# Kernel tuning notes

Measured on AMD Instinct MI355X. Metric: run time of the kernel, lower is better.

Reference implementation:

```python
import jax, jax.numpy as jnp
import numpy as np

N_DIM = 64          # n (output dim of h); d_h_in == n since traj_input=False
HIDDEN = 512        # layer_width
N_LAYERS = 3        # n_hidden_layers
BATCH = 4096


def setup_inputs() -> dict:
    key = jax.random.key(0)
    ks = jax.random.split(key, 7)
    s = 1.0 / np.sqrt(HIDDEN)
    return {
        "x": jax.random.normal(ks[0], (BATCH, 3 * N_DIM), dtype=jnp.float32),
        "W_in": jax.random.normal(ks[1], (HIDDEN, N_DIM), dtype=jnp.float32) / np.sqrt(N_DIM),
        "b_in": jax.random.normal(ks[2], (HIDDEN,), dtype=jnp.float32) * 0.01,
        "W_h": jax.random.normal(ks[3], (N_LAYERS, HIDDEN, HIDDEN), dtype=jnp.float32) * s,
        "b_h": jax.random.normal(ks[4], (N_LAYERS, HIDDEN), dtype=jnp.float32) * 0.01,
        "W_out": jax.random.normal(ks[5], (N_DIM, HIDDEN), dtype=jnp.float32) * s,
        "b_out": jax.random.normal(ks[6], (N_DIM,), dtype=jnp.float32) * 0.01,
    }


def _branch(xin, W_in, b_in, W_h, b_h, W_out, b_out):
    """Replicates the MLP forward + the module's hand-rolled Jacobian chain.
    Note: faithfully reproduces the original's delta masks, which re-apply
    layer ii to its own (already-activated) output h[ii+1]."""
    hs = [xin @ W_in.T + b_in]                      # h[0]: [B, H]
    for ii in range(N_LAYERS):
        hs.append(jax.nn.relu(hs[-1] @ W_h[ii].T + b_h[ii]))
    out = hs[-1] @ W_out.T + b_out                  # [B, n]

    g = (W_h[0] @ W_in)                             # [H, d]
    delta = (hs[1] @ W_h[0].T + b_h[0] > 0).astype(xin.dtype)  # sign(relu(.))
    g = delta[:, :, None] * g[None, :, :]           # [B, H, d]
    for ii in range(1, N_LAYERS):
        g = jnp.einsum("hk,bkd->bhd", W_h[ii], g)
        delta = (hs[ii + 1] @ W_h[ii].T + b_h[ii] > 0).astype(xin.dtype)
        g = delta[:, :, None] * g
    g = jnp.einsum("nh,bhd->bnd", W_out, g)         # [B, n, d]
    return out, g


def reference(x, W_in, b_in, W_h, b_h, W_out, b_out):
    d = N_DIM
    xt, xtdot, x_zero = x[:, :d], x[:, d:2 * d], x[:, 2 * d:]

    h_out, h_grad = _branch(xt, W_in, b_in, W_h, b_h, W_out, b_out)
    h_dot = jnp.einsum("bnd,bd->bn", h_grad, xtdot)

    _, h_zerograd = _branch(x_zero, W_in, b_in, W_h, b_h, W_out, b_out)
    h_zerograd = h_zerograd[:, :, :d]               # no-op here (d_h_in == n)
    zng = jnp.sqrt(jnp.sum(h_zerograd * h_zerograd, axis=2))  # L2 norm over dim 2

    return jnp.concatenate([h_out, h_dot, zng], axis=1)       # [B, 3n]
```

## Files before the change

kernel.cpp:

```cpp
#include <hip/hip_runtime.h>
#include <math.h>

typedef __attribute__((ext_vector_type(8))) short s8v;
typedef __attribute__((ext_vector_type(4))) short s4v;
typedef __attribute__((ext_vector_type(4))) float f4v;
typedef __attribute__((ext_vector_type(16))) float f16v;

static __device__ __forceinline__ unsigned short f2bf(float f) {
    union { float f; unsigned int u; } v; v.f = f;
    unsigned int r = v.u + 0x7fffu + ((v.u >> 16) & 1u);
    return (unsigned short)(r >> 16);
}
static __device__ __forceinline__ float bf2f(unsigned short h) {
    union { unsigned int u; float f; } t; t.u = ((unsigned int)h) << 16;
    return t.f;
}

__global__ void conv_g0(const float* __restrict__ Win, const float* __restrict__ Wh,
                        const float* __restrict__ Wout,
                        unsigned short* __restrict__ whi, unsigned short* __restrict__ wlo,
                        unsigned short* __restrict__ G0hi, unsigned short* __restrict__ G0lo,
                        unsigned short* __restrict__ G0F) {
    if (blockIdx.x < 3328) {
        int i = blockIdx.x * 256 + threadIdx.x;
        float v;
        if (i < 32768)       v = Win[i];
        else if (i < 819200) v = Wh[i - 32768];
        else                 v = Wout[i - 819200];
        unsigned short h = f2bf(v);
        whi[i] = h;
        wlo[i] = f2bf(v - bf2f(h));
    } else {
        int i = (blockIdx.x - 3328) * 4 + (threadIdx.x >> 6);
        int j = threadIdx.x & 63;
        float acc = 0.f;
        for (int k = 0; k < 512; ++k)
            acc = fmaf(Wh[i * 512 + k], Win[k * 64 + j], acc);
        unsigned short h = f2bf(acc);
        G0hi[i * 64 + j] = h;
        G0lo[i * 64 + j] = f2bf(acc - bf2f(h));
        int sl = ((i >> 4) * 2 + (j >> 5)) * 64 + (j & 31) + 32 * ((i >> 3) & 1);
        G0F[(size_t)sl * 8 + (i & 7)] = h;
    }
}


#define DF_LOAD(k0)                                                              \
    {                                                                            \
        _Pragma("unroll")                                                        \
        for (int r = 0; r < 2; ++r) {                                            \
            int idx = tid + r * 512;                                             \
            int row = idx >> 3, kq = (idx & 7) * 4;                              \
            xr[r] = *(const float4*)(X + (size_t)(m0 + row) * ldx + (k0) + kq);  \
        }                                                                        \
        {                                                                        \
            int row = tid >> 3, kq = (tid & 7) * 4;                              \
            wr = *(const float4*)(W + (size_t)(n0 + row) * ldw + (k0) + kq);     \
        }                                                                        \
    }
#define DF_STASH()                                                               \
    {                                                                            \
        _Pragma("unroll")                                                        \
        for (int r = 0; r < 2; ++r) {                                            \
            int idx = tid + r * 512;                                             \
            int row = idx >> 3, kq = (idx & 7) * 4;                              \
            Xs[kq + 0][row] = xr[r].x; Xs[kq + 1][row] = xr[r].y;                \
            Xs[kq + 2][row] = xr[r].z; Xs[kq + 3][row] = xr[r].w;                \
        }                                                                        \
        {                                                                        \
            int row = tid >> 3, kq = (tid & 7) * 4;                              \
            Ws[kq + 0][row] = wr.x; Ws[kq + 1][row] = wr.y;                      \
            Ws[kq + 2][row] = wr.z; Ws[kq + 3][row] = wr.w;                      \
        }                                                                        \
    }

static __device__ __forceinline__ void dual_fp32_body(
    unsigned char* lds, const float* __restrict__ X, int ldx,
    const float* __restrict__ W, int ldw, const float* __restrict__ bias,
    float* __restrict__ C, int ldc, unsigned char* __restrict__ maskOut,
    const unsigned char* __restrict__ maskMul, int K, int N, int mode,
    int m0, int n0)
{
    const int tid = threadIdx.x;
    float (*Xs)[132] = (float(*)[132])lds;
    float (*Ws)[68]  = (float(*)[68])(lds + 16896);
    const int tx = tid & 15, ty = tid >> 4;
    float acc[4][4] = {};
    float4 xr[2], wr;

    DF_LOAD(0);
    DF_STASH();
    __syncthreads();

    for (int k0 = 0; k0 < K; k0 += 32) {
        bool last = (k0 + 32 >= K);
        if (!last) DF_LOAD(k0 + 32);
        #pragma unroll
        for (int kk = 0; kk < 32; ++kk) {
            float4 a0 = *(const float4*)&Xs[kk][ty * 4];
            float4 b0 = *(const float4*)&Ws[kk][tx * 4];
            float av[4] = {a0.x, a0.y, a0.z, a0.w};
            float bv[4] = {b0.x, b0.y, b0.z, b0.w};
            #pragma unroll
            for (int i = 0; i < 4; ++i)
                #pragma unroll
                for (int j = 0; j < 4; ++j)
                    acc[i][j] = fmaf(av[i], bv[j], acc[i][j]);
        }
        __syncthreads();
        if (!last) {
            DF_STASH();
            __syncthreads();
        }
    }

    float4 bb = {0, 0, 0, 0};
    if (mode & 1) bb = *(const float4*)(bias + n0 + tx * 4);
    const int c0 = n0 + tx * 4;
    #pragma unroll
    for (int i = 0; i < 4; ++i) {
        int r = m0 + ty * 4 + i;
        float v[4];
        #pragma unroll
        for (int j = 0; j < 4; ++j) {
            v[j] = acc[i][j];
            if (mode & 1) v[j] += ((const float*)&bb)[j];
        }
        if (mode & 8) {
            uchar4 mo;
            mo.x = v[0] > 0.0f; mo.y = v[1] > 0.0f; mo.z = v[2] > 0.0f; mo.w = v[3] > 0.0f;
            *(uchar4*)&maskOut[(size_t)r * N + c0] = mo;
        }
        if (mode & 16) {
            uchar4 mm = *(const uchar4*)&maskMul[(size_t)r * N + c0];
            v[0] *= mm.x; v[1] *= mm.y; v[2] *= mm.z; v[3] *= mm.w;
        }
        if (mode & 2) {
            #pragma unroll
            for (int j = 0; j < 4; ++j) v[j] = fmaxf(v[j], 0.0f);
        }
        if (mode & 4) {
            float4 st = {v[0], v[1], v[2], v[3]};
            *(float4*)(C + (size_t)r * ldc + c0) = st;
        }
    }
}
#undef DF_LOAD
#undef DF_STASH

#define DM_LOAD(k0)                                                                \
    {                                                                              \
        _Pragma("unroll")                                                          \
        for (int r = 0; r < 2; ++r) {                                              \
            int idx = tid + r * 512;                                               \
            int row = idx >> 3, kq = (idx & 7) * 4;                                \
            xr[r] = *(const float4*)(X + (size_t)(m0 + row) * ldx + (k0) + kq);    \
        }                                                                          \
        if (wload) {                                                               \
            int row = tid >> 2, kc = (tid & 3) * 8;                                \
            wh = *(const s8v*)(Whi + (size_t)(n0 + row) * ldw + (k0) + kc);        \
            wl = *(const s8v*)(Wlo + (size_t)(n0 + row) * ldw + (k0) + kc);        \
        }                                                                          \
    }
#define DM_STASH()                                                                 \
    {                                                                              \
        _Pragma("unroll")                                                          \
        for (int r = 0; r < 2; ++r) {                                              \
            int idx = tid + r * 512;                                               \
            int row = idx >> 3, kq = (idx & 7) * 4;                                \
            float a[4] = {xr[r].x, xr[r].y, xr[r].z, xr[r].w};                     \
            s4v hv, lv;                                                            \
            _Pragma("unroll")                                                      \
            for (int j = 0; j < 4; ++j) {                                          \
                unsigned short h = f2bf(a[j]);                                     \
                hv[j] = (short)h;                                                  \
                lv[j] = (short)f2bf(a[j] - bf2f(h));                               \
            }                                                                      \
            *(s4v*)&Xh[row * 40 + kq] = hv;                                        \
            *(s4v*)&Xl[row * 40 + kq] = lv;                                        \
        }                                                                          \
        if (wload) {                                                               \
            int row = tid >> 2, kc = (tid & 3) * 8;                                \
            *(s8v*)&Wsh[row * 40 + kc] = wh;                                       \
            *(s8v*)&Wsl[row * 40 + kc] = wl;                                       \
        }                                                                          \
    }

static __device__ __forceinline__ void dual_mfma_body(
    unsigned char* lds, const float* __restrict__ X, int ldx,
    const unsigned short* __restrict__ Whi, const unsigned short* __restrict__ Wlo, int ldw,
    const float* __restrict__ bias, float* __restrict__ C, int ldc,
    unsigned char* __restrict__ maskOut, const unsigned char* __restrict__ maskMul,
    int K, int N, int mode, int m0, int n0)
{
    const int tid = threadIdx.x;
    unsigned short* Xh  = (unsigned short*)lds;
    unsigned short* Xl  = (unsigned short*)(lds + 10240);
    unsigned short* Wsh = (unsigned short*)(lds + 20480);
    unsigned short* Wsl = (unsigned short*)(lds + 25600);

    const int wave = tid >> 6, lane = tid & 63;
    const int q = lane >> 4, ln = lane & 15;
    const int wm = (wave & 3) * 32;
    const int wn = (wave >> 2) * 32;

    f4v acc[2][2];
    #pragma unroll
    for (int mt = 0; mt < 2; ++mt)
        #pragma unroll
        for (int nt = 0; nt < 2; ++nt)
            acc[mt][nt] = (f4v)(0.0f);

    float4 xr[2];
    s8v wh, wl;
    const bool wload = (tid < 256);

    DM_LOAD(0);
    DM_STASH();
    __syncthreads();

    for (int k0 = 0; k0 < K; k0 += 32) {
        bool last = (k0 + 32 >= K);
        if (!last) DM_LOAD(k0 + 32);

        s8v ah[2], al[2], bh[2], bl[2];
        #pragma unroll
        for (int mt = 0; mt < 2; ++mt) {
            int rowm = wm + mt * 16 + ln;
            ah[mt] = *(const s8v*)&Xh[rowm * 40 + q * 8];
            al[mt] = *(const s8v*)&Xl[rowm * 40 + q * 8];
        }
        #pragma unroll
        for (int nt = 0; nt < 2; ++nt) {
            int rown = wn + nt * 16 + ln;
            bh[nt] = *(const s8v*)&Wsh[rown * 40 + q * 8];
            bl[nt] = *(const s8v*)&Wsl[rown * 40 + q * 8];
        }
        #pragma unroll
        for (int mt = 0; mt < 2; ++mt)
            #pragma unroll
            for (int nt = 0; nt < 2; ++nt) {
                acc[mt][nt] = __builtin_amdgcn_mfma_f32_16x16x32_bf16(ah[mt], bh[nt], acc[mt][nt], 0, 0, 0);
                acc[mt][nt] = __builtin_amdgcn_mfma_f32_16x16x32_bf16(ah[mt], bl[nt], acc[mt][nt], 0, 0, 0);
                acc[mt][nt] = __builtin_amdgcn_mfma_f32_16x16x32_bf16(al[mt], bh[nt], acc[mt][nt], 0, 0, 0);
            }

        __syncthreads();
        if (!last) {
            DM_STASH();
            __syncthreads();
        }
    }

    #pragma unroll
    for (int nt = 0; nt < 2; ++nt) {
        int n = n0 + wn + nt * 16 + ln;
        float bv = (mode & 1) ? bias[n] : 0.0f;
        #pragma unroll
        for (int mt = 0; mt < 2; ++mt) {
            int mbase = m0 + wm + mt * 16 + q * 4;
            #pragma unroll
            for (int r = 0; r < 4; ++r) {
                int m = mbase + r;
                float v = acc[mt][nt][r] + bv;
                if (mode & 8)  maskOut[(size_t)m * N + n] = (v > 0.0f) ? 1 : 0;
                if (mode & 16) v *= (float)maskMul[(size_t)m * N + n];
                if (mode & 2)  v = fmaxf(v, 0.0f);
                if (mode & 4)  C[(size_t)m * ldc + n] = v;
            }
        }
    }
}
#undef DM_LOAD
#undef DM_STASH

__global__ __launch_bounds__(512) void h0_pack(
    const float* __restrict__ x, const float* __restrict__ Win,
    const unsigned short* __restrict__ WinH, const unsigned short* __restrict__ WinL,
    const float* __restrict__ bin, float* __restrict__ tA, float* __restrict__ zA,
    const unsigned short* __restrict__ whi,
    unsigned short* __restrict__ WhF, unsigned short* __restrict__ WoF)
{
    __shared__ __align__(16) unsigned char lds[30720];
    const int m0 = blockIdx.x * 128, n0 = blockIdx.y * 64;
    int z = blockIdx.z;
    if (z == 0)
        dual_fp32_body(lds, x, 192, Win, 64, bin, tA, 512, 0, 0, 64, 512, 1 | 4, m0, n0);
    else if (z == 1)
        dual_mfma_body(lds, x + 128, 192, WinH, WinL, 64, bin, zA, 512, 0, 0, 64, 512, 1 | 4, m0, n0);
    else {
        int i = (blockIdx.y * 32 + blockIdx.x) * 512 + threadIdx.x;
        if (i < 65536) {
            int lane = i & 63, ks = (i >> 6) & 31, g32 = (i >> 11) & 15, s = i >> 15;
            int row = g32 * 32 + (lane & 31);
            int k   = ks * 16 + (lane >> 5) * 8;
            const unsigned short* src = whi + 294912 + (size_t)s * 262144 + row * 512 + k;
            *(s8v*)(WhF + (size_t)i * 8) = *(const s8v*)src;
        } else if (i < 65536 + 4096) {
            int j = i - 65536;
            int lane = j & 63, ks = (j >> 6) & 31, g32 = j >> 11;
            int row = g32 * 32 + (lane & 31);
            int k   = ks * 16 + (lane >> 5) * 8;
            const unsigned short* src = whi + 819200 + row * 512 + k;
            *(s8v*)(WoF + (size_t)j * 8) = *(const s8v*)src;
        }
    }
}

__global__ __launch_bounds__(512) void gemm_dualM(
    const float* __restrict__ X0, const float* __restrict__ X1, int ldx,
    const float* __restrict__ W, int ldw,
    const unsigned short* __restrict__ Whi, const unsigned short* __restrict__ Wlo,
    const float* __restrict__ bias,
    float* __restrict__ C0, float* __restrict__ C1, int ldc,
    unsigned char* __restrict__ mo0, unsigned char* __restrict__ mo1,
    int K, int N, int mode)
{
    __shared__ __align__(16) unsigned char lds[30720];
    const int m0 = blockIdx.x * 128, n0 = blockIdx.y * 64;
    if (blockIdx.z == 0)
        dual_fp32_body(lds, X0, ldx, W, ldw, bias, C0, ldc, mo0, 0, K, N, mode, m0, n0);
    else
        dual_mfma_body(lds, X1, ldx, Whi, Wlo, ldw, bias, C1, ldc, mo1, 0, K, N, mode, m0, n0);
}

__global__ __launch_bounds__(512) void gemm_dual4(
    const float* __restrict__ X0, const float* __restrict__ X1, int ldx,
    const float* __restrict__ Wn, const float* __restrict__ Wd, int ldw,
    const unsigned short* __restrict__ WnH, const unsigned short* __restrict__ WnL,
    const unsigned short* __restrict__ WdH, const unsigned short* __restrict__ WdL,
    const float* __restrict__ bn, const float* __restrict__ bd,
    float* __restrict__ C0, float* __restrict__ C1, int ldc,
    unsigned char* __restrict__ mot, unsigned char* __restrict__ moz,
    int K, int N)
{
    __shared__ __align__(16) unsigned char lds[30720];
    const int m0 = blockIdx.x * 128, n0 = blockIdx.y * 64;
    int z = blockIdx.z;
    if (z == 0)
        dual_fp32_body(lds, X0, ldx, Wn, ldw, bn, C0, ldc, 0, 0, K, N, 1 | 2 | 4, m0, n0);
    else if (z == 2)
        dual_fp32_body(lds, X0, ldx, Wd, ldw, bd, 0, ldc, mot, 0, K, N, 1 | 8, m0, n0);
    else if (z == 1)
        dual_mfma_body(lds, X1, ldx, WnH, WnL, ldw, bn, C1, ldc, 0, 0, K, N, 1 | 2 | 4, m0, n0);
    else
        dual_mfma_body(lds, X1, ldx, WdH, WdL, ldw, bd, 0, ldc, moz, 0, K, N, 1 | 8, m0, n0);
}

__global__ __launch_bounds__(512) void d3v1(
    const float* __restrict__ tB, const float* __restrict__ zB, const float* __restrict__ x,
    const float* __restrict__ Wh2,
    const unsigned short* __restrict__ Wh2H, const unsigned short* __restrict__ Wh2L,
    const unsigned short* __restrict__ G0hi, const unsigned short* __restrict__ G0lo,
    const float* __restrict__ bh2, float* __restrict__ tA,
    unsigned char* __restrict__ mt3, unsigned char* __restrict__ mz3,
    const unsigned char* __restrict__ mt1)
{
    __shared__ __align__(16) unsigned char lds[30720];
    const int m0 = blockIdx.x * 128, n0 = blockIdx.y * 64;
    int z = blockIdx.z;
    if (z == 0)
        dual_fp32_body(lds, tB, 512, Wh2, 512, bh2, 0, 512, mt3, 0, 512, 512, 1 | 8, m0, n0);
    else if (z == 1)
        dual_mfma_body(lds, zB, 512, Wh2H, Wh2L, 512, bh2, 0, 512, mz3, 0, 512, 512, 1 | 8, m0, n0);
    else
        dual_mfma_body(lds, x + 64, 192, G0hi, G0lo, 64, 0, tA, 512, 0, mt1, 64, 512, 4 | 16, m0, n0);
}

__global__ __launch_bounds__(512) void gemm_m1(
    const float* __restrict__ X, int ldx,
    const unsigned short* __restrict__ Whi, const unsigned short* __restrict__ Wlo, int ldw,
    float* __restrict__ C, int ldc,
    const unsigned char* __restrict__ maskMul,
    int K, int N, int mode)
{
    __shared__ __align__(16) unsigned char lds[30720];
    dual_mfma_body(lds, X, ldx, Whi, Wlo, ldw, 0, C, ldc, 0, maskMul, K, N, mode,
                   blockIdx.x * 128, blockIdx.y * 64);
}

__global__ __launch_bounds__(512) void gemm_mm(
    const float* __restrict__ X0, const float* __restrict__ X1, int ldx,
    const unsigned short* __restrict__ Whi, const unsigned short* __restrict__ Wlo, int ldw,
    const float* __restrict__ bias,
    float* __restrict__ C0, float* __restrict__ C1, int ldc,
    int K, int N, int mode0, int mode1)
{
    __shared__ __align__(16) unsigned char lds[30720];
    const int m0 = blockIdx.x * 128, n0 = blockIdx.y * 64;
    if (blockIdx.z == 0)
        dual_mfma_body(lds, X0, ldx, Whi, Wlo, ldw, bias, C0, ldc, 0, 0, K, N, mode0, m0, n0);
    else
        dual_mfma_body(lds, X1, ldx, Whi, Wlo, ldw, bias, C1, ldc, 0, 0, K, N, mode1, m0, n0);
}

__global__ __launch_bounds__(512, 4) void zng_v2(
    const unsigned short* __restrict__ WhF,
    const unsigned short* __restrict__ WoF,
    const unsigned short* __restrict__ G0F,
    const unsigned char* __restrict__ mz1,
    const unsigned char* __restrict__ mz2,
    const unsigned char* __restrict__ mz3,
    float* __restrict__ out,
    const float* __restrict__ tA,
    const unsigned short* __restrict__ Wh1H, const unsigned short* __restrict__ Wh1L,
    const unsigned char* __restrict__ mt2,
    float* __restrict__ zA)
{
    __shared__ __align__(16) unsigned char ldsb[66560];

    if (blockIdx.x >= 4096) {
        int idx = blockIdx.x - 4096;
        dual_mfma_body(ldsb, tA, 512, Wh1H, Wh1L, 512, 0, zA, 512, 0, mt2,
                       512, 512, 4 | 16, (idx & 31) * 128, (idx >> 5) * 64);
        return;
    }

    unsigned short* RtF = (unsigned short*)ldsb;
    unsigned char* m2s = ldsb + 65536;
    unsigned char* m3s = ldsb + 66048;

    const int b0  = blockIdx.x;
    const int tid = threadIdx.x;

    m2s[tid] = mz2[(size_t)b0 * 512 + tid];
    m3s[tid] = mz3[(size_t)b0 * 512 + tid];

    #pragma unroll
    for (int it = 0; it < 8; ++it) {
        int sl = it * 512 + tid;
        int ls = sl & 63;
        int ks = sl >> 7;
        int k0 = ks * 16 + (ls >> 5) * 8;
        s8v g = *(const s8v*)(G0F + (size_t)sl * 8);
        const unsigned char* mm = mz1 + (size_t)b0 * 512 + k0;
        unsigned int mlo = *(const unsigned int*)(mm);
        unsigned int mhi = *(const unsigned int*)(mm + 4);
        s8v r;
        #pragma unroll
        for (int j = 0; j < 4; ++j) r[j] = ((mlo >> (8 * j)) & 1) ? g[j] : (short)0;
        #pragma unroll
        for (int j = 0; j < 4; ++j) r[4 + j] = ((mhi >> (8 * j)) & 1) ? g[4 + j] : (short)0;
        *(s8v*)(&RtF[(size_t)sl * 8]) = r;
    }
    __syncthreads();

    const int lane = tid & 63, wave = tid >> 6;
    const int l31 = lane & 31, h = lane >> 5;

    for (int s = 0; s < 2; ++s) {
        const unsigned short* Ar0 = WhF + (size_t)s * 262144
                                  + (size_t)(wave * 2) * 16384 + lane * 8;
        const unsigned short* Ar1 = Ar0 + 16384;

        f16v acc[2][2];
        #pragma unroll
        for (int mt = 0; mt < 2; ++mt)
            #pragma unroll
            for (int nt = 0; nt < 2; ++nt)
                acc[mt][nt] = (f16v)(0.0f);

        s8v a0A = *(const s8v*)(Ar0);
        s8v a1A = *(const s8v*)(Ar1);
        s8v a0B = *(const s8v*)(Ar0 + 512);
        s8v a1B = *(const s8v*)(Ar1 + 512);
        s8v b0c = *(const s8v*)&RtF[lane * 8];
        s8v b1c = *(const s8v*)&RtF[512 + lane * 8];

        #pragma unroll 4
        for (int ks = 0; ks < 32; ++ks) {
            int kf = ((ks + 2) & 31) * 512;
            s8v a0N = *(const s8v*)(Ar0 + kf);
            s8v a1N = *(const s8v*)(Ar1 + kf);
            int kb = ((ks + 1) & 31) * 1024;
            s8v b0n = *(const s8v*)&RtF[kb + lane * 8];
            s8v b1n = *(const s8v*)&RtF[kb + 512 + lane * 8];

            __builtin_amdgcn_s_setprio(1);
            acc[0][0] = __builtin_amdgcn_mfma_f32_32x32x16_bf16(a0A, b0c, acc[0][0], 0, 0, 0);
            acc[0][1] = __builtin_amdgcn_mfma_f32_32x32x16_bf16(a0A, b1c, acc[0][1], 0, 0, 0);
            acc[1][0] = __builtin_amdgcn_mfma_f32_32x32x16_bf16(a1A, b0c, acc[1][0], 0, 0, 0);
            acc[1][1] = __builtin_amdgcn_mfma_f32_32x32x16_bf16(a1A, b1c, acc[1][1], 0, 0, 0);
            __builtin_amdgcn_s_setprio(0);

            a0A = a0B; a0B = a0N;
            a1A = a1B; a1B = a1N;
            b0c = b0n; b1c = b1n;
        }
        __syncthreads();

        const unsigned char* msk = (s == 0) ? m2s : m3s;
        #pragma unroll
        for (int mt = 0; mt < 2; ++mt) {
            #pragma unroll
            for (int g = 0; g < 4; ++g) {
                int kk = wave * 64 + mt * 32 + g * 8 + h * 4;
                int ks = wave * 4 + mt * 2 + (g >> 1);
                int khalf = g & 1;
                uchar4 mv = *(const uchar4*)&msk[kk];
                unsigned char mb[4] = {mv.x, mv.y, mv.z, mv.w};
                #pragma unroll
                for (int nt = 0; nt < 2; ++nt) {
                    s4v pk;
                    #pragma unroll
                    for (int r = 0; r < 4; ++r) {
                        float v = mb[r] ? acc[mt][nt][g * 4 + r] : 0.0f;
                        pk[r] = (short)f2bf(v);
                    }
                    *(s4v*)(&RtF[(ks * 2 + nt) * 512 + (l31 + 32 * khalf) * 8 + h * 4]) = pk;
                }
            }
        }
        __syncthreads();
    }

    if (wave < 2) {
        const unsigned short* Wr = WoF + wave * 16384 + lane * 8;
        f16v a3[2];
        a3[0] = (f16v)(0.0f);
        a3[1] = (f16v)(0.0f);
        #pragma unroll 2
        for (int ks = 0; ks < 32; ++ks) {
            s8v af = *(const s8v*)(Wr + ks * 512);
            s8v bb0 = *(const s8v*)&RtF[ks * 1024 + lane * 8];
            s8v bb1 = *(const s8v*)&RtF[ks * 1024 + 512 + lane * 8];
            a3[0] = __builtin_amdgcn_mfma_f32_32x32x16_bf16(af, bb0, a3[0], 0, 0, 0);
            a3[1] = __builtin_amdgcn_mfma_f32_32x32x16_bf16(af, bb1, a3[1], 0, 0, 0);
        }
        float sq[16];
        #pragma unroll
        for (int i = 0; i < 16; ++i) {
            float v0 = a3[0][i], v1 = a3[1][i];
            sq[i] = fmaf(v0, v0, v1 * v1);
        }
        #pragma unroll
        for (int off = 1; off < 32; off <<= 1)
            #pragma unroll
            for (int i = 0; i < 16; ++i)
                sq[i] += __shfl_xor(sq[i], off, 64);
        if (l31 == 0) {
            #pragma unroll
            for (int g = 0; g < 4; ++g)
                #pragma unroll
                for (int r = 0; r < 4; ++r)
                    out[(size_t)b0 * 192 + 128 + wave * 32 + g * 8 + h * 4 + r] = sqrtf(sq[g * 4 + r]);
        }
    }
}

extern "C" void kernel_launch(void* const* d_in, const int* in_sizes, int n_in,
                              void* d_out, int out_size, void* d_ws, size_t ws_size,
                              hipStream_t stream) {
    const float* x    = (const float*)d_in[0];
    const float* Win  = (const float*)d_in[1];
    const float* bin  = (const float*)d_in[2];
    const float* Wh   = (const float*)d_in[3];
    const float* bh   = (const float*)d_in[4];
    const float* Wout = (const float*)d_in[5];
    const float* bout = (const float*)d_in[6];
    float* out = (float*)d_out;

    char* ws = (char*)d_ws;
    unsigned short* whi  = (unsigned short*)(ws);
    unsigned short* wlo  = (unsigned short*)(ws + 1703936);
    unsigned short* G0hi = (unsigned short*)(ws + 3407872);
    unsigned short* G0lo = (unsigned short*)(ws + 3473408);
    unsigned short* G0F  = (unsigned short*)(ws + 3538944);
    unsigned char*  masks = (unsigned char*)(ws + 3604480);
    unsigned char* mt1 = masks + 0 * 2097152;
    unsigned char* mt2 = masks + 1 * 2097152;
    unsigned char* mt3 = masks + 2 * 2097152;
    unsigned char* mz1 = masks + 3 * 2097152;
    unsigned char* mz2 = masks + 4 * 2097152;
    unsigned char* mz3 = masks + 5 * 2097152;
    float* bufs = (float*)(ws + 3604480 + 12582912);
    float* tA = bufs + 0 * 2097152;
    float* tB = bufs + 1 * 2097152;
    float* zA = bufs + 2 * 2097152;
    float* zB = bufs + 3 * 2097152;
    unsigned short* WhF = (unsigned short*)(ws + 49741824);
    unsigned short* WoF = (unsigned short*)(ws + 50790400);

    const unsigned short* WinH  = whi,          *WinL  = wlo;
    const unsigned short* Wh0H  = whi + 32768,  *Wh0L  = wlo + 32768;
    const unsigned short* Wh1H  = whi + 294912, *Wh1L  = wlo + 294912;
    const unsigned short* Wh2H  = whi + 557056, *Wh2L  = wlo + 557056;
    const unsigned short* WoutH = whi + 819200, *WoutL = wlo + 819200;

    const float* Wh0 = Wh;
    const float* Wh1 = Wh + 262144;
    const float* Wh2 = Wh + 524288;
    const float* bh0 = bh, *bh1 = bh + 512, *bh2 = bh + 1024;

    conv_g0<<<dim3(3456), dim3(256), 0, stream>>>(Win, Wh, Wout, whi, wlo, G0hi, G0lo, G0F);
    h0_pack<<<dim3(32, 8, 3), dim3(512), 0, stream>>>(x, Win, WinH, WinL, bin, tA, zA,
                                                      whi, WhF, WoF);

    gemm_dualM<<<dim3(32, 8, 2), dim3(512), 0, stream>>>(tA, zA, 512, Wh0, 512, Wh0H, Wh0L, bh0,
                                                         tB, zB, 512, 0, 0, 512, 512, 1 | 2 | 4);
    gemm_dual4<<<dim3(32, 8, 4), dim3(512), 0, stream>>>(tB, zB, 512, Wh1, Wh0, 512,
                                                         Wh1H, Wh1L, Wh0H, Wh0L, bh1, bh0,
                                                         tA, zA, 512, mt1, mz1, 512, 512);
    gemm_dual4<<<dim3(32, 8, 4), dim3(512), 0, stream>>>(tA, zA, 512, Wh2, Wh1, 512,
                                                         Wh2H, Wh2L, Wh1H, Wh1L, bh2, bh1,
                                                         tB, zB, 512, mt2, mz2, 512, 512);
    d3v1<<<dim3(32, 8, 3), dim3(512), 0, stream>>>(tB, zB, x, Wh2, Wh2H, Wh2L, G0hi, G0lo,
                                                   bh2, tA, mt3, mz3, mt1);

    zng_v2<<<dim3(4352), dim3(512), 0, stream>>>(WhF, WoF, G0F, mz1, mz2, mz3, out,
                                                 tA, Wh1H, Wh1L, mt2, zA);

    gemm_m1<<<dim3(32, 8), dim3(512), 0, stream>>>(zA, 512, Wh2H, Wh2L, 512, zB, 512,
                                                   mt3, 512, 512, 4 | 16);

    gemm_mm<<<dim3(32, 1, 2), dim3(512), 0, stream>>>(tB, zB, 512, WoutH, WoutL, 512, bout,
                                                      out, out + 64, 192, 512, 64, 1 | 4, 4);
}
```

Before: 662.0 us.

## Process two batch rows per zng block to reuse weight fragments

The per-sample Jacobian-norm kernel now handles two batch samples per 512-thread block. Each group of four waves owns one sample and computes 128 rows of the 512x64 product with four M-tiles, so every loaded weight fragment feeds twice as many MFMAs. LDS per block doubles to about 130 KB and the launch-bounds occupancy hint drops from 4 to 2, which cuts resident waves and raises register pressure in exchange for halving global weight traffic per sample.

```diff
diff --git a/kernel.cpp b/kernel.cpp
--- a/kernel.cpp
+++ b/kernel.cpp
@@ -394,7 +394,7 @@
         dual_mfma_body(lds, X1, ldx, Whi, Wlo, ldw, bias, C1, ldc, 0, 0, K, N, mode1, m0, n0);
 }
 
-__global__ __launch_bounds__(512, 4) void zng_v2(
+__global__ __launch_bounds__(512, 2) void zng_v2(
     const unsigned short* __restrict__ WhF,
     const unsigned short* __restrict__ WoF,
     const unsigned short* __restrict__ G0F,
@@ -407,95 +407,113 @@
     const unsigned char* __restrict__ mt2,
     float* __restrict__ zA)
 {
-    __shared__ __align__(16) unsigned char ldsb[66560];
-
-    if (blockIdx.x >= 4096) {
-        int idx = blockIdx.x - 4096;
+    __shared__ __align__(16) unsigned char ldsb[133120];
+
+    if (blockIdx.x >= 2048) {
+        int idx = blockIdx.x - 2048;
         dual_mfma_body(ldsb, tA, 512, Wh1H, Wh1L, 512, 0, zA, 512, 0, mt2,
                        512, 512, 4 | 16, (idx & 31) * 128, (idx >> 5) * 64);
         return;
     }
 
-    unsigned short* RtF = (unsigned short*)ldsb;
-    unsigned char* m2s = ldsb + 65536;
-    unsigned char* m3s = ldsb + 66048;
+    unsigned short* RtF0 = (unsigned short*)ldsb;
+    unsigned short* RtF1 = (unsigned short*)(ldsb + 65536);
+    unsigned char* m2s = ldsb + 131072;
+    unsigned char* m3s = ldsb + 132096;
 
     const int b0  = blockIdx.x;
     const int tid = threadIdx.x;
 
-    m2s[tid] = mz2[(size_t)b0 * 512 + tid];
-    m3s[tid] = mz3[(size_t)b0 * 512 + tid];
-
     #pragma unroll
-    for (int it = 0; it < 8; ++it) {
-        int sl = it * 512 + tid;
-        int ls = sl & 63;
-        int ks = sl >> 7;
-        int k0 = ks * 16 + (ls >> 5) * 8;
-        s8v g = *(const s8v*)(G0F + (size_t)sl * 8);
-        const unsigned char* mm = mz1 + (size_t)b0 * 512 + k0;
-        unsigned int mlo = *(const unsigned int*)(mm);
-        unsigned int mhi = *(const unsigned int*)(mm + 4);
-        s8v r;
-        #pragma unroll
-        for (int j = 0; j < 4; ++j) r[j] = ((mlo >> (8 * j)) & 1) ? g[j] : (short)0;
-        #pragma unroll
-        for (int j = 0; j < 4; ++j) r[4 + j] = ((mhi >> (8 * j)) & 1) ? g[4 + j] : (short)0;
-        *(s8v*)(&RtF[(size_t)sl * 8]) = r;
+    for (int e = 0; e < 2; ++e) {
+        m2s[e * 512 + tid] = mz2[(size_t)(2 * b0 + e) * 512 + tid];
+        m3s[e * 512 + tid] = mz3[(size_t)(2 * b0 + e) * 512 + tid];
+    }
+
+    {
+        const int e = tid >> 8, t256 = tid & 255;
+        unsigned short* RtF = e ? RtF1 : RtF0;
+        const unsigned char* mme = mz1 + (size_t)(2 * b0 + e) * 512;
+        #pragma unroll
+        for (int it = 0; it < 16; ++it) {
+            int sl = it * 256 + t256;
+            int ls = sl & 63;
+            int ks = sl >> 7;
+            int k0 = ks * 16 + (ls >> 5) * 8;
+            s8v g = *(const s8v*)(G0F + (size_t)sl * 8);
+            unsigned int mlo = *(const unsigned int*)(mme + k0);
+            unsigned int mhi = *(const unsigned int*)(mme + k0 + 4);
+            s8v r;
+            #pragma unroll
+            for (int j = 0; j < 4; ++j) r[j] = ((mlo >> (8 * j)) & 1) ? g[j] : (short)0;
+            #pragma unroll
+            for (int j = 0; j < 4; ++j) r[4 + j] = ((mhi >> (8 * j)) & 1) ? g[4 + j] : (short)0;
+            *(s8v*)(&RtF[(size_t)sl * 8]) = r;
+        }
     }
     __syncthreads();
 
     const int lane = tid & 63, wave = tid >> 6;
     const int l31 = lane & 31, h = lane >> 5;
+    const int we = wave >> 2;
+    const int wq = wave & 3;
+    unsigned short* RtF = we ? RtF1 : RtF0;
 
     for (int s = 0; s < 2; ++s) {
-        const unsigned short* Ar0 = WhF + (size_t)s * 262144
-                                  + (size_t)(wave * 2) * 16384 + lane * 8;
-        const unsigned short* Ar1 = Ar0 + 16384;
-
-        f16v acc[2][2];
-        #pragma unroll
-        for (int mt = 0; mt < 2; ++mt)
+        const unsigned short* Ar = WhF + (size_t)s * 262144
+                                 + (size_t)(wq * 4) * 16384 + lane * 8;
+
+        f16v acc[4][2];
+        #pragma unroll
+        for (int mt = 0; mt < 4; ++mt)
             #pragma unroll
             for (int nt = 0; nt < 2; ++nt)
                 acc[mt][nt] = (f16v)(0.0f);
 
-        s8v a0A = *(const s8v*)(Ar0);
-        s8v a1A = *(const s8v*)(Ar1);
-        s8v a0B = *(const s8v*)(Ar0 + 512);
-        s8v a1B = *(const s8v*)(Ar1 + 512);
+        s8v aA[4], aB[4];
+        #pragma unroll
+        for (int mt = 0; mt < 4; ++mt) {
+            aA[mt] = *(const s8v*)(Ar + (size_t)mt * 16384);
+            aB[mt] = *(const s8v*)(Ar + (size_t)mt * 16384 + 512);
+        }
         s8v b0c = *(const s8v*)&RtF[lane * 8];
         s8v b1c = *(const s8v*)&RtF[512 + lane * 8];
 
         #pragma unroll 4
         for (int ks = 0; ks < 32; ++ks) {
             int kf = ((ks + 2) & 31) * 512;
-            s8v a0N = *(const s8v*)(Ar0 + kf);
-            s8v a1N = *(const s8v*)(Ar1 + kf);
+            s8v aN[4];
+            #pragma unroll
+            for (int mt = 0; mt < 4; ++mt)
+                aN[mt] = *(const s8v*)(Ar + (size_t)mt * 16384 + kf);
             int kb = ((ks + 1) & 31) * 1024;
             s8v b0n = *(const s8v*)&RtF[kb + lane * 8];
             s8v b1n = *(const s8v*)&RtF[kb + 512 + lane * 8];
 
             __builtin_amdgcn_s_setprio(1);
-            acc[0][0] = __builtin_amdgcn_mfma_f32_32x32x16_bf16(a0A, b0c, acc[0][0], 0, 0, 0);
-            acc[0][1] = __builtin_amdgcn_mfma_f32_32x32x16_bf16(a0A, b1c, acc[0][1], 0, 0, 0);
-            acc[1][0] = __builtin_amdgcn_mfma_f32_32x32x16_bf16(a1A, b0c, acc[1][0], 0, 0, 0);
-            acc[1][1] = __builtin_amdgcn_mfma_f32_32x32x16_bf16(a1A, b1c, acc[1][1], 0, 0, 0);
+            #pragma unroll
+            for (int mt = 0; mt < 4; ++mt) {
+                acc[mt][0] = __builtin_amdgcn_mfma_f32_32x32x16_bf16(aA[mt], b0c, acc[mt][0], 0, 0, 0);
+                acc[mt][1] = __builtin_amdgcn_mfma_f32_32x32x16_bf16(aA[mt], b1c, acc[mt][1], 0, 0, 0);
+            }
             __builtin_amdgcn_s_setprio(0);
 
-            a0A = a0B; a0B = a0N;
-            a1A = a1B; a1B = a1N;
+            #pragma unroll
+            for (int mt = 0; mt < 4; ++mt) {
+                aA[mt] = aB[mt];
+                aB[mt] = aN[mt];
+            }
             b0c = b0n; b1c = b1n;
         }
         __syncthreads();
 
-        const unsigned char* msk = (s == 0) ? m2s : m3s;
-        #pragma unroll
-        for (int mt = 0; mt < 2; ++mt) {
+        const unsigned char* msk = ((s == 0) ? m2s : m3s) + we * 512;
+        #pragma unroll
+        for (int mt = 0; mt < 4; ++mt) {
             #pragma unroll
             for (int g = 0; g < 4; ++g) {
-                int kk = wave * 64 + mt * 32 + g * 8 + h * 4;
-                int ks = wave * 4 + mt * 2 + (g >> 1);
+                int kk = wq * 128 + mt * 32 + g * 8 + h * 4;
+                int ks2 = wq * 8 + mt * 2 + (g >> 1);
                 int khalf = g & 1;
                 uchar4 mv = *(const uchar4*)&msk[kk];
                 unsigned char mb[4] = {mv.x, mv.y, mv.z, mv.w};
@@ -507,15 +525,15 @@
                         float v = mb[r] ? acc[mt][nt][g * 4 + r] : 0.0f;
                         pk[r] = (short)f2bf(v);
                     }
-                    *(s4v*)(&RtF[(ks * 2 + nt) * 512 + (l31 + 32 * khalf) * 8 + h * 4]) = pk;
+                    *(s4v*)(&RtF[(ks2 * 2 + nt) * 512 + (l31 + 32 * khalf) * 8 + h * 4]) = pk;
                 }
             }
         }
         __syncthreads();
     }
 
-    if (wave < 2) {
-        const unsigned short* Wr = WoF + wave * 16384 + lane * 8;
+    if (wq < 2) {
+        const unsigned short* Wr = WoF + wq * 16384 + lane * 8;
         f16v a3[2];
         a3[0] = (f16v)(0.0f);
         a3[1] = (f16v)(0.0f);
@@ -543,7 +561,7 @@
             for (int g = 0; g < 4; ++g)
                 #pragma unroll
                 for (int r = 0; r < 4; ++r)
-                    out[(size_t)b0 * 192 + 128 + wave * 32 + g * 8 + h * 4 + r] = sqrtf(sq[g * 4 + r]);
+                    out[(size_t)(2 * b0 + we) * 192 + 128 + wq * 32 + g * 8 + h * 4 + r] = sqrtf(sq[g * 4 + r]);
         }
     }
 }
@@ -607,7 +625,7 @@
     d3v1<<<dim3(32, 8, 3), dim3(512), 0, stream>>>(tB, zB, x, Wh2, Wh2H, Wh2L, G0hi, G0lo,
                                                    bh2, tA, mt3, mz3, mt1);
 
-    zng_v2<<<dim3(4352), dim3(512), 0, stream>>>(WhF, WoF, G0F, mz1, mz2, mz3, out,
+    zng_v2<<<dim3(2304), dim3(512), 0, stream>>>(WhF, WoF, G0F, mz1, mz2, mz3, out,
                                                  tA, Wh1H, Wh1L, mt2, zA);
 
     gemm_m1<<<dim3(32, 8), dim3(512), 0, stream>>>(zA, 512, Wh2H, Wh2L, 512, zB, 512,
```

Result: slower. 698.5 us (+5.5%).

## Store intermediate activations as pre-split bf16 hi/lo pairs between GEMM stages

Applied to the files above, without the earlier changes.

Producer GEMM epilogues now write bf16 hi/lo split pairs instead of fp32 for the activation and tangent buffers consumed by split-bf16 MFMA GEMMs. A new pp_mfma_body loads these pre-split operands directly, which removes the per-tile fp32-to-bf16 split work in the load path. Global traffic per element stays the same (two shorts instead of one float), but the split conversion moves from every consumer tile into one producer epilogue. The scalar 2-byte epilogue stores may be less coalesced than the previous 4-byte stores.

```diff
diff --git a/kernel.cpp b/kernel.cpp
--- a/kernel.cpp
+++ b/kernel.cpp
@@ -148,6 +148,37 @@
 #undef DF_LOAD
 #undef DF_STASH
 
+static __device__ __forceinline__ void mfma_epi(
+    f4v (&acc)[2][2], const float* __restrict__ bias,
+    float* __restrict__ C, unsigned short* __restrict__ Ch, unsigned short* __restrict__ Cl,
+    int ldc, unsigned char* __restrict__ maskOut, const unsigned char* __restrict__ maskMul,
+    int N, int mode, int m0, int n0, int wm, int wn, int q, int ln)
+{
+    #pragma unroll
+    for (int nt = 0; nt < 2; ++nt) {
+        int n = n0 + wn + nt * 16 + ln;
+        float bv = (mode & 1) ? bias[n] : 0.0f;
+        #pragma unroll
+        for (int mt = 0; mt < 2; ++mt) {
+            int mbase = m0 + wm + mt * 16 + q * 4;
+            #pragma unroll
+            for (int r = 0; r < 4; ++r) {
+                int m = mbase + r;
+                float v = acc[mt][nt][r] + bv;
+                if (mode & 8)  maskOut[(size_t)m * N + n] = (v > 0.0f) ? 1 : 0;
+                if (mode & 16) v *= (float)maskMul[(size_t)m * N + n];
+                if (mode & 2)  v = fmaxf(v, 0.0f);
+                if (mode & 4)  C[(size_t)m * ldc + n] = v;
+                if (mode & 32) {
+                    unsigned short hh = f2bf(v);
+                    Ch[(size_t)m * ldc + n] = hh;
+                    Cl[(size_t)m * ldc + n] = f2bf(v - bf2f(hh));
+                }
+            }
+        }
+    }
+}
+
 #define DM_LOAD(k0)                                                                \
     {                                                                              \
         _Pragma("unroll")                                                          \
@@ -189,8 +220,9 @@
 static __device__ __forceinline__ void dual_mfma_body(
     unsigned char* lds, const float* __restrict__ X, int ldx,
     const unsigned short* __restrict__ Whi, const unsigned short* __restrict__ Wlo, int ldw,
-    const float* __restrict__ bias, float* __restrict__ C, int ldc,
-    unsigned char* __restrict__ maskOut, const unsigned char* __restrict__ maskMul,
+    const float* __restrict__ bias,
+    float* __restrict__ C, unsigned short* __restrict__ Ch, unsigned short* __restrict__ Cl,
+    int ldc, unsigned char* __restrict__ maskOut, const unsigned char* __restrict__ maskMul,
     int K, int N, int mode, int m0, int n0)
 {
     const int tid = threadIdx.x;
@@ -252,32 +284,109 @@
         }
     }
 
-    #pragma unroll
-    for (int nt = 0; nt < 2; ++nt) {
-        int n = n0 + wn + nt * 16 + ln;
-        float bv = (mode & 1) ? bias[n] : 0.0f;
-        #pragma unroll
-        for (int mt = 0; mt < 2; ++mt) {
-            int mbase = m0 + wm + mt * 16 + q * 4;
-            #pragma unroll
-            for (int r = 0; r < 4; ++r) {
-                int m = mbase + r;
-                float v = acc[mt][nt][r] + bv;
-                if (mode & 8)  maskOut[(size_t)m * N + n] = (v > 0.0f) ? 1 : 0;
-                if (mode & 16) v *= (float)maskMul[(size_t)m * N + n];
-                if (mode & 2)  v = fmaxf(v, 0.0f);
-                if (mode & 4)  C[(size_t)m * ldc + n] = v;
-            }
-        }
-    }
+    mfma_epi(acc, bias, C, Ch, Cl, ldc, maskOut, maskMul, N, mode, m0, n0, wm, wn, q, ln);
 }
 #undef DM_LOAD
 #undef DM_STASH
+
+#define PP_LOAD(k0)                                                                \
+    {                                                                              \
+        int row = tid >> 2, kc = (tid & 3) * 8;                                    \
+        xh8 = *(const s8v*)(Xhg + (size_t)(m0 + row) * ldx + (k0) + kc);           \
+        xl8 = *(const s8v*)(Xlg + (size_t)(m0 + row) * ldx + (k0) + kc);           \
+        if (wload) {                                                               \
+            wh = *(const s8v*)(Whi + (size_t)(n0 + row) * ldw + (k0) + kc);        \
+            wl = *(const s8v*)(Wlo + (size_t)(n0 + row) * ldw + (k0) + kc);        \
+        }                                                                          \
+    }
+#define PP_STASH()                                                                 \
+    {                                                                              \
+        int row = tid >> 2, kc = (tid & 3) * 8;                                    \
+        *(s8v*)&Xh[row * 40 + kc] = xh8;                                           \
+        *(s8v*)&Xl[row * 40 + kc] = xl8;                                           \
+        if (wload) {                                                               \
+            *(s8v*)&Wsh[row * 40 + kc] = wh;                                       \
+            *(s8v*)&Wsl[row * 40 + kc] = wl;                                       \
+        }                                                                          \
+    }
+
+static __device__ __forceinline__ void pp_mfma_body(
+    unsigned char* lds,
+    const unsigned short* __restrict__ Xhg, const unsigned short* __restrict__ Xlg, int ldx,
+    const unsigned short* __restrict__ Whi, const unsigned short* __restrict__ Wlo, int ldw,
+    const float* __restrict__ bias,
+    float* __restrict__ C, unsigned short* __restrict__ Ch, unsigned short* __restrict__ Cl,
+    int ldc, unsigned char* __restrict__ maskOut, const unsigned char* __restrict__ maskMul,
+    int K, int N, int mode, int m0, int n0)
+{
+    const int tid = threadIdx.x;
+    unsigned short* Xh  = (unsigned short*)lds;
+    unsigned short* Xl  = (unsigned short*)(lds + 10240);
+    unsigned short* Wsh = (unsigned short*)(lds + 20480);
+    unsigned short* Wsl = (unsigned short*)(lds + 25600);
+
+    const int wave = tid >> 6, lane = tid & 63;
+    const int q = lane >> 4, ln = lane & 15;
+    const int wm = (wave & 3) * 32;
+    const int wn = (wave >> 2) * 32;
+
+    f4v acc[2][2];
+    #pragma unroll
+    for (int mt = 0; mt < 2; ++mt)
+        #pragma unroll
+        for (int nt = 0; nt < 2; ++nt)
+            acc[mt][nt] = (f4v)(0.0f);
+
+    s8v xh8, xl8, wh, wl;
+    const bool wload = (tid < 256);
+
+    PP_LOAD(0);
+    PP_STASH();
+    __syncthreads();
+
+    for (int k0 = 0; k0 < K; k0 += 32) {
+        bool last = (k0 + 32 >= K);
+        if (!last) PP_LOAD(k0 + 32);
+
+        s8v ah[2], al[2], bh[2], bl[2];
+        #pragma unroll
+        for (int mt = 0; mt < 2; ++mt) {
+            int rowm = wm + mt * 16 + ln;
+            ah[mt] = *(const s8v*)&Xh[rowm * 40 + q * 8];
+            al[mt] = *(const s8v*)&Xl[rowm * 40 + q * 8];
+        }
+        #pragma unroll
+        for (int nt = 0; nt < 2; ++nt) {
+            int rown = wn + nt * 16 + ln;
+            bh[nt] = *(const s8v*)&Wsh[rown * 40 + q * 8];
+            bl[nt] = *(const s8v*)&Wsl[rown * 40 + q * 8];
+        }
+        #pragma unroll
+        for (int mt = 0; mt < 2; ++mt)
+            #pragma unroll
+            for (int nt = 0; nt < 2; ++nt) {
+                acc[mt][nt] = __builtin_amdgcn_mfma_f32_16x16x32_bf16(ah[mt], bh[nt], acc[mt][nt], 0, 0, 0);
+                acc[mt][nt] = __builtin_amdgcn_mfma_f32_16x16x32_bf16(ah[mt], bl[nt], acc[mt][nt], 0, 0, 0);
+                acc[mt][nt] = __builtin_amdgcn_mfma_f32_16x16x32_bf16(al[mt], bh[nt], acc[mt][nt], 0, 0, 0);
+            }
+
+        __syncthreads();
+        if (!last) {
+            PP_STASH();
+            __syncthreads();
+        }
+    }
+
+    mfma_epi(acc, bias, C, Ch, Cl, ldc, maskOut, maskMul, N, mode, m0, n0, wm, wn, q, ln);
+}
+#undef PP_LOAD
+#undef PP_STASH
 
 __global__ __launch_bounds__(512) void h0_pack(
     const float* __restrict__ x, const float* __restrict__ Win,
     const unsigned short* __restrict__ WinH, const unsigned short* __restrict__ WinL,
-    const float* __restrict__ bin, float* __restrict__ tA, float* __restrict__ zA,
+    const float* __restrict__ bin, float* __restrict__ tA,
+    unsigned short* __restrict__ zAh, unsigned short* __restrict__ zAl,
     const unsigned short* __restrict__ whi,
     unsigned short* __restrict__ WhF, unsigned short* __restrict__ WoF)
 {
@@ -287,7 +396,8 @@
     if (z == 0)
         dual_fp32_body(lds, x, 192, Win, 64, bin, tA, 512, 0, 0, 64, 512, 1 | 4, m0, n0);
     else if (z == 1)
-        dual_mfma_body(lds, x + 128, 192, WinH, WinL, 64, bin, zA, 512, 0, 0, 64, 512, 1 | 4, m0, n0);
+        dual_mfma_body(lds, x + 128, 192, WinH, WinL, 64, bin, 0, zAh, zAl, 512, 0, 0,
+                       64, 512, 1 | 32, m0, n0);
     else {
         int i = (blockIdx.y * 32 + blockIdx.x) * 512 + threadIdx.x;
         if (i < 65536) {
@@ -308,51 +418,58 @@
 }
 
 __global__ __launch_bounds__(512) void gemm_dualM(
-    const float* __restrict__ X0, const float* __restrict__ X1, int ldx,
-    const float* __restrict__ W, int ldw,
+    const float* __restrict__ X0,
+    const unsigned short* __restrict__ X1h, const unsigned short* __restrict__ X1l,
+    const float* __restrict__ W,
     const unsigned short* __restrict__ Whi, const unsigned short* __restrict__ Wlo,
     const float* __restrict__ bias,
-    float* __restrict__ C0, float* __restrict__ C1, int ldc,
-    unsigned char* __restrict__ mo0, unsigned char* __restrict__ mo1,
-    int K, int N, int mode)
+    float* __restrict__ C0,
+    unsigned short* __restrict__ C1h, unsigned short* __restrict__ C1l)
 {
     __shared__ __align__(16) unsigned char lds[30720];
     const int m0 = blockIdx.x * 128, n0 = blockIdx.y * 64;
     if (blockIdx.z == 0)
-        dual_fp32_body(lds, X0, ldx, W, ldw, bias, C0, ldc, mo0, 0, K, N, mode, m0, n0);
+        dual_fp32_body(lds, X0, 512, W, 512, bias, C0, 512, 0, 0, 512, 512, 1 | 2 | 4, m0, n0);
     else
-        dual_mfma_body(lds, X1, ldx, Whi, Wlo, ldw, bias, C1, ldc, mo1, 0, K, N, mode, m0, n0);
+        pp_mfma_body(lds, X1h, X1l, 512, Whi, Wlo, 512, bias, 0, C1h, C1l, 512, 0, 0,
+                     512, 512, 1 | 2 | 32, m0, n0);
 }
 
 __global__ __launch_bounds__(512) void gemm_dual4(
-    const float* __restrict__ X0, const float* __restrict__ X1, int ldx,
-    const float* __restrict__ Wn, const float* __restrict__ Wd, int ldw,
+    const float* __restrict__ X0,
+    const unsigned short* __restrict__ X1h, const unsigned short* __restrict__ X1l,
+    const float* __restrict__ Wn, const float* __restrict__ Wd,
     const unsigned short* __restrict__ WnH, const unsigned short* __restrict__ WnL,
     const unsigned short* __restrict__ WdH, const unsigned short* __restrict__ WdL,
     const float* __restrict__ bn, const float* __restrict__ bd,
-    float* __restrict__ C0, float* __restrict__ C1, int ldc,
-    unsigned char* __restrict__ mot, unsigned char* __restrict__ moz,
-    int K, int N)
+    float* __restrict__ C0,
+    unsigned short* __restrict__ C1h, unsigned short* __restrict__ C1l,
+    unsigned char* __restrict__ mot, unsigned char* __restrict__ moz)
 {
     __shared__ __align__(16) unsigned char lds[30720];
     const int m0 = blockIdx.x * 128, n0 = blockIdx.y * 64;
     int z = blockIdx.z;
     if (z == 0)
-        dual_fp32_body(lds, X0, ldx, Wn, ldw, bn, C0, ldc, 0, 0, K, N, 1 | 2 | 4, m0, n0);
+        dual_fp32_body(lds, X0, 512, Wn, 512, bn, C0, 512, 0, 0, 512, 512, 1 | 2 | 4, m0, n0);
     else if (z == 2)
-        dual_fp32_body(lds, X0, ldx, Wd, ldw, bd, 0, ldc, mot, 0, K, N, 1 | 8, m0, n0);
+        dual_fp32_body(lds, X0, 512, Wd, 512, bd, 0, 512, mot, 0, 512, 512, 1 | 8, m0, n0);
     else if (z == 1)
-        dual_mfma_body(lds, X1, ldx, WnH, WnL, ldw, bn, C1, ldc, 0, 0, K, N, 1 | 2 | 4, m0, n0);
+        pp_mfma_body(lds, X1h, X1l, 512, WnH, WnL, 512, bn, 0, C1h, C1l, 512, 0, 0,
+                     512, 512, 1 | 2 | 32, m0, n0);
     else
-        dual_mfma_body(lds, X1, ldx, WdH, WdL, ldw, bd, 0, ldc, moz, 0, K, N, 1 | 8, m0, n0);
+        pp_mfma_body(lds, X1h, X1l, 512, WdH, WdL, 512, bd, 0, 0, 0, 512, moz, 0,
+                     512, 512, 1 | 8, m0, n0);
 }
 
 __global__ __launch_bounds__(512) void d3v1(
-    const float* __restrict__ tB, const float* __restrict__ zB, const float* __restrict__ x,
+    const float* __restrict__ tB,
+    const unsigned short* __restrict__ zBh, const unsigned short* __restrict__ zBl,
+    const float* __restrict__ x,
     const float* __restrict__ Wh2,
     const unsigned short* __restrict__ Wh2H, const unsigned short* __restrict__ Wh2L,
     const unsigned short* __restrict__ G0hi, const unsigned short* __restrict__ G0lo,
-    const float* __restrict__ bh2, float* __restrict__ tA,
+    const float* __restrict__ bh2,
+    unsigned short* __restrict__ tAh, unsigned short* __restrict__ tAl,
     unsigned char* __restrict__ mt3, unsigned char* __restrict__ mz3,
     const unsigned char* __restrict__ mt1)
 {
@@ -362,36 +479,38 @@
     if (z == 0)
         dual_fp32_body(lds, tB, 512, Wh2, 512, bh2, 0, 512, mt3, 0, 512, 512, 1 | 8, m0, n0);
     else if (z == 1)
-        dual_mfma_body(lds, zB, 512, Wh2H, Wh2L, 512, bh2, 0, 512, mz3, 0, 512, 512, 1 | 8, m0, n0);
+        pp_mfma_body(lds, zBh, zBl, 512, Wh2H, Wh2L, 512, bh2, 0, 0, 0, 512, mz3, 0,
+                     512, 512, 1 | 8, m0, n0);
     else
-        dual_mfma_body(lds, x + 64, 192, G0hi, G0lo, 64, 0, tA, 512, 0, mt1, 64, 512, 4 | 16, m0, n0);
-}
-
-__global__ __launch_bounds__(512) void gemm_m1(
-    const float* __restrict__ X, int ldx,
-    const unsigned short* __restrict__ Whi, const unsigned short* __restrict__ Wlo, int ldw,
-    float* __restrict__ C, int ldc,
-    const unsigned char* __restrict__ maskMul,
-    int K, int N, int mode)
+        dual_mfma_body(lds, x + 64, 192, G0hi, G0lo, 64, 0, 0, tAh, tAl, 512, 0, mt1,
+                       64, 512, 32 | 16, m0, n0);
+}
+
+__global__ __launch_bounds__(512) void gemm_v3(
+    const unsigned short* __restrict__ Xh, const unsigned short* __restrict__ Xl,
+    const unsigned short* __restrict__ Whi, const unsigned short* __restrict__ Wlo,
+    unsigned short* __restrict__ Ch, unsigned short* __restrict__ Cl,
+    const unsigned char* __restrict__ maskMul)
 {
     __shared__ __align__(16) unsigned char lds[30720];
-    dual_mfma_body(lds, X, ldx, Whi, Wlo, ldw, 0, C, ldc, 0, maskMul, K, N, mode,
-                   blockIdx.x * 128, blockIdx.y * 64);
+    pp_mfma_body(lds, Xh, Xl, 512, Whi, Wlo, 512, 0, 0, Ch, Cl, 512, 0, maskMul,
+                 512, 512, 32 | 16, blockIdx.x * 128, blockIdx.y * 64);
 }
 
 __global__ __launch_bounds__(512) void gemm_mm(
-    const float* __restrict__ X0, const float* __restrict__ X1, int ldx,
-    const unsigned short* __restrict__ Whi, const unsigned short* __restrict__ Wlo, int ldw,
-    const float* __restrict__ bias,
-    float* __restrict__ C0, float* __restrict__ C1, int ldc,
-    int K, int N, int mode0, int mode1)
+    const float* __restrict__ tB,
+    const unsigned short* __restrict__ zBh, const unsigned short* __restrict__ zBl,
+    const unsigned short* __restrict__ Whi, const unsigned short* __restrict__ Wlo,
+    const float* __restrict__ bias, float* __restrict__ out)
 {
     __shared__ __align__(16) unsigned char lds[30720];
     const int m0 = blockIdx.x * 128, n0 = blockIdx.y * 64;
     if (blockIdx.z == 0)
-        dual_mfma_body(lds, X0, ldx, Whi, Wlo, ldw, bias, C0, ldc, 0, 0, K, N, mode0, m0, n0);
+        dual_mfma_body(lds, tB, 512, Whi, Wlo, 512, bias, out, 0, 0, 192, 0, 0,
+                       512, 64, 1 | 4, m0, n0);
     else
-        dual_mfma_body(lds, X1, ldx, Whi, Wlo, ldw, bias, C1, ldc, 0, 0, K, N, mode1, m0, n0);
+        pp_mfma_body(lds, zBh, zBl, 512, Whi, Wlo, 512, 0, out + 64, 0, 0, 192, 0, 0,
+                     512, 64, 4, m0, n0);
 }
 
 __global__ __launch_bounds__(512, 4) void zng_v2(
@@ -402,17 +521,17 @@
     const unsigned char* __restrict__ mz2,
     const unsigned char* __restrict__ mz3,
     float* __restrict__ out,
-    const float* __restrict__ tA,
+    const unsigned short* __restrict__ tAh, const unsigned short* __restrict__ tAl,
     const unsigned short* __restrict__ Wh1H, const unsigned short* __restrict__ Wh1L,
     const unsigned char* __restrict__ mt2,
-    float* __restrict__ zA)
+    unsigned short* __restrict__ zAh, unsigned short* __restrict__ zAl)
 {
     __shared__ __align__(16) unsigned char ldsb[66560];
 
     if (blockIdx.x >= 4096) {
         int idx = blockIdx.x - 4096;
-        dual_mfma_body(ldsb, tA, 512, Wh1H, Wh1L, 512, 0, zA, 512, 0, mt2,
-                       512, 512, 4 | 16, (idx & 31) * 128, (idx >> 5) * 64);
+        pp_mfma_body(ldsb, tAh, tAl, 512, Wh1H, Wh1L, 512, 0, 0, zAh, zAl, 512, 0, mt2,
+                     512, 512, 32 | 16, (idx & 31) * 128, (idx >> 5) * 64);
         return;
     }
 
@@ -576,8 +695,12 @@
     float* bufs = (float*)(ws + 3604480 + 12582912);
     float* tA = bufs + 0 * 2097152;
     float* tB = bufs + 1 * 2097152;
-    float* zA = bufs + 2 * 2097152;
-    float* zB = bufs + 3 * 2097152;
+    unsigned short* zAh = (unsigned short*)(bufs + 2 * 2097152);
+    unsigned short* zAl = zAh + 2097152;
+    unsigned short* zBh = (unsigned short*)(bufs + 3 * 2097152);
+    unsigned short* zBl = zBh + 2097152;
+    unsigned short* tAh = (unsigned short*)tA;
+    unsigned short* tAl = tAh + 2097152;
     unsigned short* WhF = (unsigned short*)(ws + 49741824);
     unsigned short* WoF = (unsigned short*)(ws + 50790400);
 
@@ -593,26 +716,25 @@
     const float* bh0 = bh, *bh1 = bh + 512, *bh2 = bh + 1024;
 
     conv_g0<<<dim3(3456), dim3(256), 0, stream>>>(Win, Wh, Wout, whi, wlo, G0hi, G0lo, G0F);
-    h0_pack<<<dim3(32, 8, 3), dim3(512), 0, stream>>>(x, Win, WinH, WinL, bin, tA, zA,
+    h0_pack<<<dim3(32, 8, 3), dim3(512), 0, stream>>>(x, Win, WinH, WinL, bin, tA, zAh, zAl,
                                                       whi, WhF, WoF);
 
-    gemm_dualM<<<dim3(32, 8, 2), dim3(512), 0, stream>>>(tA, zA, 512, Wh0, 512, Wh0H, Wh0L, bh0,
-                                                         tB, zB, 512, 0, 0, 512, 512, 1 | 2 | 4);
-    gemm_dual4<<<dim3(32, 8, 4), dim3(512), 0, stream>>>(tB, zB, 512, Wh1, Wh0, 512,
+    gemm_dualM<<<dim3(32, 8, 2), dim3(512), 0, stream>>>(tA, zAh, zAl, Wh0, Wh0H, Wh0L, bh0,
+                                                         tB, zBh, zBl);
+    gemm_dual4<<<dim3(32, 8, 4), dim3(512), 0, stream>>>(tB, zBh, zBl, Wh1, Wh0,
                                                          Wh1H, Wh1L, Wh0H, Wh0L, bh1, bh0,
-                                                         tA, zA, 512, mt1, mz1, 512, 512);
-    gemm_dual4<<<dim3(32, 8, 4), dim3(512), 0, stream>>>(tA, zA, 512, Wh2, Wh1, 512,
+                                                         tA, zAh, zAl, mt1, mz1);
+    gemm_dual4<<<dim3(32, 8, 4), dim3(512), 0, stream>>>(tA, zAh, zAl, Wh2, Wh1,
                                                          Wh2H, Wh2L, Wh1H, Wh1L, bh2, bh1,
-                                                         tB, zB, 512, mt2, mz2, 512, 512);
-    d3v1<<<dim3(32, 8, 3), dim3(512), 0, stream>>>(tB, zB, x, Wh2, Wh2H, Wh2L, G0hi, G0lo,
-                                                   bh2, tA, mt3, mz3, mt1);
+                                                         tB, zBh, zBl, mt2, mz2);
+    d3v1<<<dim3(32, 8, 3), dim3(512), 0, stream>>>(tB, zBh, zBl, x, Wh2, Wh2H, Wh2L,
+                                                   G0hi, G0lo, bh2, tAh, tAl,
+                                                   mt3, mz3, mt1);
 
     zng_v2<<<dim3(4352), dim3(512), 0, stream>>>(WhF, WoF, G0F, mz1, mz2, mz3, out,
-                                                 tA, Wh1H, Wh1L, mt2, zA);
-
-    gemm_m1<<<dim3(32, 8), dim3(512), 0, stream>>>(zA, 512, Wh2H, Wh2L, 512, zB, 512,
-                                                   mt3, 512, 512, 4 | 16);
-
-    gemm_mm<<<dim3(32, 1, 2), dim3(512), 0, stream>>>(tB, zB, 512, WoutH, WoutL, 512, bout,
-                                                      out, out + 64, 192, 512, 64, 1 | 4, 4);
-}
+                                                 tAh, tAl, Wh1H, Wh1L, mt2, zAh, zAl);
+
+    gemm_v3<<<dim3(32, 8), dim3(512), 0, stream>>>(zAh, zAl, Wh2H, Wh2L, zBh, zBl, mt3);
+
+    gemm_mm<<<dim3(32, 1, 2), dim3(512), 0, stream>>>(tB, zBh, zBl, WoutH, WoutL, bout, out);
+}
```

Result: faster. 623.8 us (median of 3 runs) (-5.8%).
